# Kernel optimization log

Measured on AMD Instinct MI355X. Metric: run time of the kernel, lower is better.

The kernel has to match this reference:

```python
import jax, jax.numpy as jnp
import numpy as np

BS, C, D = 4096, 16384, 128
POS_ALPHA, POS_DELTA = 32.0, 0.1
NEG_ALPHA, NEG_DELTA = 32.0, -0.1


def _normalize(x):
    # F.normalize(x, dim=1)
    return x / jnp.linalg.norm(x, axis=1, keepdims=True)


def _masked_lse(sims, mask, axis, use_max):
    """Faithful port of Criterion.masked_logsumexp (returns per-entry lse and the
    nonzero-entry mask that torch uses to filter before the final mean)."""
    m = sims * mask
    if use_max:
        ref = jnp.max(m, axis=axis, keepdims=True)
    else:
        ref = jnp.min(m, axis=axis, keepdims=True)
    ref = jax.lax.stop_gradient(ref)  # torch: ref_v.detach()
    # torch: nz_entries = max + min of (sims*mask); keep where nonzero
    nz = (jnp.max(m, axis=axis) + jnp.min(m, axis=axis)) != 0
    s = jnp.sum(jnp.exp(sims - ref) * mask, axis=axis)
    lse = jnp.log(jnp.where(nz, s, 1.0)) + jnp.squeeze(ref, axis=axis)
    return lse, nz


def setup_inputs() -> dict:
    key = jax.random.key(0)
    k1, k2, k3 = jax.random.split(key, 3)
    batch = jax.random.normal(k1, (BS, D), dtype=jnp.float32)
    # proxies = randn/proxy_div, init_dev=0 so no max-shift
    proxies = jax.random.normal(k2, (C, D), dtype=jnp.float32) / 8.0
    labels = jax.random.randint(k3, (BS,), 0, C)
    return {"batch": batch, "proxies": proxies, "labels": labels}


def reference(batch, proxies, labels):
    batch = _normalize(batch)          # [BS, D]
    proxies = _normalize(proxies)      # [C, D]

    pos_sims = batch @ proxies[labels].T   # [BS, BS] cosine sims to positive proxies
    sims = batch @ proxies.T               # [BS, C]

    same = (labels[:, None] == labels[None, :]).astype(batch.dtype)              # [BS, BS]
    diff = (labels[:, None] != jnp.arange(C)[None, :]).astype(batch.dtype)       # [BS, C]

    w_pos = -POS_ALPHA * (pos_sims - POS_DELTA)
    w_neg = NEG_ALPHA * (sims - NEG_DELTA)

    # mode='anchor' -> dim=0; cosine -> max=False for pos, max=True for neg
    pos_lse, pos_nz = _masked_lse(w_pos, same, axis=0, use_max=False)
    neg_lse, neg_nz = _masked_lse(w_neg, diff, axis=0, use_max=True)

    # nca_clean=False -> softplus
    pos_s = jax.nn.softplus(pos_lse)
    neg_s = jax.nn.softplus(neg_lse)

    # torch takes mean only over nz entries
    pos_mean = jnp.sum(jnp.where(pos_nz, pos_s, 0.0)) / jnp.maximum(jnp.sum(pos_nz), 1).astype(batch.dtype)
    neg_mean = jnp.sum(jnp.where(neg_nz, neg_s, 0.0)) / jnp.maximum(jnp.sum(neg_nz), 1).astype(batch.dtype)
    return pos_mean + neg_mean
```

## Files before the change

### kernel.cpp

```cpp
#include <hip/hip_runtime.h>
#include <math.h>

#define BS 4096
#define C_CLS 16384
#define D 128
#define NS 32
#define NR 2
#define KE 46.16624130844683f
#define POS_C 4.616624130844683f
#define LN2 0.69314718055994531f
#define CORR_BLOCKS 256
#define NEG_BLOCKS 2048

typedef __attribute__((ext_vector_type(8))) short short8;
typedef __attribute__((ext_vector_type(4))) float f32x4;

__device__ inline float bf2f(unsigned short h) {
    return __uint_as_float(((unsigned)h) << 16);
}
__device__ inline unsigned short f2bf(float f) {
    unsigned u = __float_as_uint(f);
    u += 0x7FFF + ((u >> 16) & 1);
    return (unsigned short)(u >> 16);
}
__device__ inline float fastexp2(float x) {
    return __int_as_float((int)fmaf(x, 8388608.0f, 1064866816.0f));
}
__device__ inline float softplus(float x) {
    return fmaxf(x, 0.0f) + log1pf(__expf(-fabsf(x)));
}
__device__ inline void gload16(const void* g, void* l) {
    __builtin_amdgcn_global_load_lds((const __attribute__((address_space(1))) void*)g,
                                     (__attribute__((address_space(3))) void*)l, 16, 0, 0);
}
__device__ inline unsigned fenc(float f) {
    unsigned u = __float_as_uint(f);
    return (u & 0x80000000u) ? ~u : (u | 0x80000000u);
}
__device__ inline float fdec(unsigned k) {
    return (k & 0x80000000u) ? __uint_as_float(k ^ 0x80000000u) : __uint_as_float(~k);
}

__global__ __launch_bounds__(256) void normalize_all(const float* __restrict__ batch,
                                                     const float* __restrict__ proxies,
                                                     short* __restrict__ bbf,
                                                     short* __restrict__ pbf,
                                                     float* __restrict__ acc,
                                                     float* __restrict__ negSub,
                                                     float* __restrict__ posSum,
                                                     float* __restrict__ posCnt,
                                                     unsigned* __restrict__ posMaxK,
                                                     unsigned* __restrict__ posMinK,
                                                     float* __restrict__ negAcc,
                                                     int* __restrict__ counter) {
    const int sub = threadIdx.x >> 5;
    const int lane32 = threadIdx.x & 31;
    const int row = blockIdx.x * 8 + sub;
    const bool isb = row < BS;
    const float* src = isb ? batch : proxies;
    short* dst = isb ? bbf : pbf;
    const int r = isb ? row : row - BS;
    const float sc = isb ? 1.0f : KE;

    float4 v = ((const float4*)(src + (size_t)r * D))[lane32];
    float ss = v.x * v.x + v.y * v.y + v.z * v.z + v.w * v.w;
#pragma unroll
    for (int off = 16; off; off >>= 1) ss += __shfl_xor(ss, off);
    float inv = rsqrtf(ss) * sc;
    ushort4 o;
    o.x = f2bf(v.x * inv);
    o.y = f2bf(v.y * inv);
    o.z = f2bf(v.z * inv);
    o.w = f2bf(v.w * inv);
    ((ushort4*)(dst + (size_t)r * D))[lane32] = o;

    const int bid = blockIdx.x, t = threadIdx.x;
    if (bid < 64) negSub[bid * 256 + t] = 0.0f;
    else if (bid < 128) posSum[(bid - 64) * 256 + t] = 0.0f;
    else if (bid < 192) posCnt[(bid - 128) * 256 + t] = 0.0f;
    else if (bid < 256) posMaxK[(bid - 192) * 256 + t] = 0u;
    else if (bid < 320) posMinK[(bid - 256) * 256 + t] = 0xFFFFFFFFu;
    else if (bid < 384) negAcc[(bid - 320) * 256 + t] = 0.0f;
    if (bid == 0 && t == 0) *counter = 0;
}

__global__ __launch_bounds__(256) void mm_all(const short* __restrict__ pbf,
                                              const short* __restrict__ bbf,
                                              const int* __restrict__ labels,
                                              float* __restrict__ negSub,
                                              float* __restrict__ posSum,
                                              float* __restrict__ posCnt,
                                              unsigned* __restrict__ posMaxK,
                                              unsigned* __restrict__ posMinK,
                                              float* __restrict__ negAcc) {
    __shared__ short8 frag[2][16 * 64];

    const int bid = blockIdx.x;
    const int tid = threadIdx.x;
    const int w = tid >> 6, lane = tid & 63, l16 = lane & 15, g = lane >> 4;

    if (bid < CORR_BLOCKS) {
        const int ibase = bid * 16 + w * 4;
        int lab[4];
        float d[4];
#pragma unroll
        for (int r = 0; r < 4; r++) {
            const int i = ibase + r;
            lab[r] = labels[i];
            ushort2 av = ((const ushort2*)(bbf + (size_t)i * D))[lane];
            ushort2 pv = ((const ushort2*)(pbf + (size_t)lab[r] * D))[lane];
            d[r] = bf2f(av.x) * bf2f(pv.x) + bf2f(av.y) * bf2f(pv.y);
        }
#pragma unroll
        for (int off = 32; off; off >>= 1)
#pragma unroll
            for (int r = 0; r < 4; r++) d[r] += __shfl_xor(d[r], off);

        if (lane == 0) {
#pragma unroll
            for (int r = 0; r < 4; r++) {
                atomicAdd(&negSub[lab[r]], fastexp2(d[r]));
                atomicAdd(&posSum[lab[r]], fastexp2(POS_C - d[r]));
                atomicAdd(&posCnt[lab[r]], 1.0f);
                unsigned k = fenc(fmaf(d[r], -LN2, 3.2f));
                atomicMax(&posMaxK[lab[r]], k);
                atomicMin(&posMinK[lab[r]], k);
            }
        }
        return;
    }

    const int n = bid - CORR_BLOCKS;
    const int pg = (n & 7) * 8 + ((n >> 3) & 7);
    const int sp = n >> 6;
    const int wbase = pg * 256 + w * 64;

    short8 a[4][4];
#pragma unroll
    for (int pt = 0; pt < 4; pt++)
#pragma unroll
        for (int kk = 0; kk < 4; kk++)
            a[pt][kk] = *(const short8*)(pbf + (size_t)(wbase + pt * 16 + l16) * D + kk * 32 + g * 8);

    float s[4][4];
#pragma unroll
    for (int pt = 0; pt < 4; pt++)
#pragma unroll
        for (int r = 0; r < 4; r++) s[pt][r] = 0.0f;

    const int ibeg = sp * (BS / NS);
    const short* srcbase = bbf + (size_t)(ibeg + w * 16 + l16) * D + g * 8;

#define STAGE(rr)                                                            \
    {                                                                        \
        const short* sn_ = srcbase + (size_t)(rr) * 64 * D;                  \
        _Pragma("unroll") for (int kk = 0; kk < 4; kk++)                     \
            gload16(sn_ + kk * 32, &frag[(rr) & 1][(w * 4 + kk) * 64]);      \
    }

    STAGE(0)
    asm volatile("s_waitcnt vmcnt(0)" ::: "memory");
    __syncthreads();

#pragma unroll
    for (int rnd = 0; rnd < NR; rnd++) {
        if (rnd + 1 < NR) STAGE(rnd + 1)

        const short8* fb = &frag[rnd & 1][0];
#pragma unroll
        for (int bt = 0; bt < 4; bt++) {
            short8 b[4];
#pragma unroll
            for (int kk = 0; kk < 4; kk++) b[kk] = fb[(bt * 4 + kk) * 64 + lane];
#pragma unroll
            for (int pt = 0; pt < 4; pt++) {
                f32x4 acc = {0.0f, 0.0f, 0.0f, 0.0f};
#pragma unroll
                for (int kk = 0; kk < 4; kk++)
                    acc = __builtin_amdgcn_mfma_f32_16x16x32_bf16(a[pt][kk], b[kk], acc, 0, 0, 0);
#pragma unroll
                for (int r = 0; r < 4; r++) s[pt][r] += fastexp2(acc[r]);
            }
        }
        asm volatile("s_waitcnt vmcnt(0)" ::: "memory");
        __syncthreads();
    }
#undef STAGE

#pragma unroll
    for (int off = 1; off < 16; off <<= 1)
#pragma unroll
        for (int pt = 0; pt < 4; pt++)
#pragma unroll
            for (int r = 0; r < 4; r++) s[pt][r] += __shfl_xor(s[pt][r], off);

    if (l16 == 0) {
#pragma unroll
        for (int pt = 0; pt < 4; pt++)
#pragma unroll
            for (int r = 0; r < 4; r++)
                atomicAdd(&negAcc[wbase + pt * 16 + g * 4 + r], s[pt][r]);
    }
}

__global__ __launch_bounds__(256) void final_reduce(const float* __restrict__ negAcc,
                                                    const float* __restrict__ negSub,
                                                    const int* __restrict__ labels,
                                                    const float* __restrict__ posSum,
                                                    const float* __restrict__ posCnt,
                                                    const unsigned* __restrict__ posMaxK,
                                                    const unsigned* __restrict__ posMinK,
                                                    float* __restrict__ acc,
                                                    int* __restrict__ counter,
                                                    float* __restrict__ out) {
    const int n = blockIdx.x * 256 + threadIdx.x;
    float add = 0.0f, cnt = 0.0f;
    int slot;
    if (n < C_CLS) {
        slot = 2;
        float s = fmaxf(negAcc[n] - negSub[n], 1e-30f);
        add = softplus(logf(s) + 3.2f);
        cnt = 1.0f;
    } else {
        slot = 0;
        const int j = n - C_CLS;
        const int lab = labels[j];
        float s = posSum[lab], c = posCnt[lab];
        float mxw = fdec(posMaxK[lab]), mnw = fdec(posMinK[lab]);
        float maxm = (c < (float)BS) ? fmaxf(mxw, 0.0f) : mxw;
        float minm = (c < (float)BS) ? fminf(mnw, 0.0f) : mnw;
        bool nz = (maxm + minm) != 0.0f;
        if (nz) {
            add = softplus(logf(s));
            cnt = 1.0f;
        }
    }
#pragma unroll
    for (int off = 32; off; off >>= 1) {
        add += __shfl_xor(add, off);
        cnt += __shfl_xor(cnt, off);
    }
    if ((threadIdx.x & 63) == 0) {
        atomicAdd(&acc[slot], add);
        atomicAdd(&acc[slot + 1], cnt);
    }

    __shared__ int amLast;
    __threadfence();
    if (threadIdx.x == 0) amLast = (atomicAdd(counter, 1) == (int)gridDim.x - 1);
    __syncthreads();
    if (amLast && threadIdx.x == 0) {
        __threadfence();
        out[0] = acc[0] / fmaxf(acc[1], 1.0f) + acc[2] / fmaxf(acc[3], 1.0f);
    }
}

extern "C" void kernel_launch(void* const* d_in, const int* in_sizes, int n_in,
                              void* d_out, int out_size, void* d_ws, size_t ws_size,
                              hipStream_t stream) {
    const float* batch = (const float*)d_in[0];
    const float* proxies = (const float*)d_in[1];
    const int* labels = (const int*)d_in[2];
    float* out = (float*)d_out;

    char* ws = (char*)d_ws;
    float* acc = (float*)ws;
    int* counter = (int*)(ws + 64);
    short* bbf = (short*)(ws + 256);
    short* pbf = (short*)(ws + 256 + (size_t)BS * D * 2);
    char* p = ws + 256 + (size_t)(BS + C_CLS) * D * 2;
    float* negSub = (float*)p;        p += (size_t)C_CLS * 4;
    float* posSum = (float*)p;        p += (size_t)C_CLS * 4;
    float* posCnt = (float*)p;        p += (size_t)C_CLS * 4;
    unsigned* posMaxK = (unsigned*)p; p += (size_t)C_CLS * 4;
    unsigned* posMinK = (unsigned*)p; p += (size_t)C_CLS * 4;
    float* negAcc = (float*)p;

    normalize_all<<<(BS + C_CLS) / 8, 256, 0, stream>>>(batch, proxies, bbf, pbf, acc,
                                                        negSub, posSum, posCnt, posMaxK,
                                                        posMinK, negAcc, counter);
    mm_all<<<CORR_BLOCKS + NEG_BLOCKS, 256, 0, stream>>>(pbf, bbf, labels, negSub,
                                                         posSum, posCnt, posMaxK,
                                                         posMinK, negAcc);
    final_reduce<<<(C_CLS + BS) / 256, 256, 0, stream>>>(negAcc, negSub, labels, posSum,
                                                         posCnt, posMaxK, posMinK,
                                                         acc, counter, out);
}
```

Baseline: 51.63 us.

## Replace atomic neg accumulation with per-split partial buffer and fewer, longer blocks

The batch dimension in the negative-sum GEMM is split into 8 slices instead of 32, so each block loops over 8 staged rounds and there are 512 negative blocks instead of 2048. Each slice now writes its per-class partial exp-sums to its own row of a partial buffer instead of using global atomicAdd. The final reduce kernel sums the 8 partials per class. This removes atomic contention and the zero-init of the accumulator, and amortizes the A-fragment loads over more rounds. The cost is fewer blocks to fill the GPU and a non-unrolled round loop.

```diff
diff --git a/kernel.cpp b/kernel.cpp
--- a/kernel.cpp
+++ b/kernel.cpp
@@ -4,13 +4,13 @@
 #define BS 4096
 #define C_CLS 16384
 #define D 128
-#define NS 32
-#define NR 2
+#define NS 8
+#define NR 8
 #define KE 46.16624130844683f
 #define POS_C 4.616624130844683f
 #define LN2 0.69314718055994531f
 #define CORR_BLOCKS 256
-#define NEG_BLOCKS 2048
+#define NEG_BLOCKS 512
 
 typedef __attribute__((ext_vector_type(8))) short short8;
 typedef __attribute__((ext_vector_type(4))) float f32x4;
@@ -51,7 +51,6 @@
                                                      float* __restrict__ posCnt,
                                                      unsigned* __restrict__ posMaxK,
                                                      unsigned* __restrict__ posMinK,
-                                                     float* __restrict__ negAcc,
                                                      int* __restrict__ counter) {
     const int sub = threadIdx.x >> 5;
     const int lane32 = threadIdx.x & 31;
@@ -80,19 +79,18 @@
     else if (bid < 192) posCnt[(bid - 128) * 256 + t] = 0.0f;
     else if (bid < 256) posMaxK[(bid - 192) * 256 + t] = 0u;
     else if (bid < 320) posMinK[(bid - 256) * 256 + t] = 0xFFFFFFFFu;
-    else if (bid < 384) negAcc[(bid - 320) * 256 + t] = 0.0f;
     if (bid == 0 && t == 0) *counter = 0;
 }
 
 __global__ __launch_bounds__(256) void mm_all(const short* __restrict__ pbf,
                                               const short* __restrict__ bbf,
                                               const int* __restrict__ labels,
+                                              float* __restrict__ S,
                                               float* __restrict__ negSub,
                                               float* __restrict__ posSum,
                                               float* __restrict__ posCnt,
                                               unsigned* __restrict__ posMaxK,
-                                              unsigned* __restrict__ posMinK,
-                                              float* __restrict__ negAcc) {
+                                              unsigned* __restrict__ posMinK) {
     __shared__ short8 frag[2][16 * 64];
 
     const int bid = blockIdx.x;
@@ -162,11 +160,11 @@
     asm volatile("s_waitcnt vmcnt(0)" ::: "memory");
     __syncthreads();
 
-#pragma unroll
     for (int rnd = 0; rnd < NR; rnd++) {
+        const int cur = rnd & 1;
         if (rnd + 1 < NR) STAGE(rnd + 1)
 
-        const short8* fb = &frag[rnd & 1][0];
+        const short8* fb = &frag[cur][0];
 #pragma unroll
         for (int bt = 0; bt < 4; bt++) {
             short8 b[4];
@@ -198,12 +196,14 @@
 #pragma unroll
         for (int pt = 0; pt < 4; pt++)
 #pragma unroll
-            for (int r = 0; r < 4; r++)
-                atomicAdd(&negAcc[wbase + pt * 16 + g * 4 + r], s[pt][r]);
-    }
-}
-
-__global__ __launch_bounds__(256) void final_reduce(const float* __restrict__ negAcc,
+            for (int r = 0; r < 4; r++) {
+                int row = wbase + pt * 16 + g * 4 + r;
+                S[(size_t)sp * C_CLS + row] = s[pt][r];
+            }
+    }
+}
+
+__global__ __launch_bounds__(256) void final_reduce(const float* __restrict__ S,
                                                     const float* __restrict__ negSub,
                                                     const int* __restrict__ labels,
                                                     const float* __restrict__ posSum,
@@ -218,7 +218,10 @@
     int slot;
     if (n < C_CLS) {
         slot = 2;
-        float s = fmaxf(negAcc[n] - negSub[n], 1e-30f);
+        float s = 0.0f;
+#pragma unroll
+        for (int p = 0; p < NS; p++) s += S[(size_t)p * C_CLS + n];
+        s = fmaxf(s - negSub[n], 1e-30f);
         add = softplus(logf(s) + 3.2f);
         cnt = 1.0f;
     } else {
@@ -269,20 +272,19 @@
     short* bbf = (short*)(ws + 256);
     short* pbf = (short*)(ws + 256 + (size_t)BS * D * 2);
     char* p = ws + 256 + (size_t)(BS + C_CLS) * D * 2;
+    float* negS = (float*)p;          p += (size_t)C_CLS * NS * 4;
     float* negSub = (float*)p;        p += (size_t)C_CLS * 4;
     float* posSum = (float*)p;        p += (size_t)C_CLS * 4;
     float* posCnt = (float*)p;        p += (size_t)C_CLS * 4;
     unsigned* posMaxK = (unsigned*)p; p += (size_t)C_CLS * 4;
-    unsigned* posMinK = (unsigned*)p; p += (size_t)C_CLS * 4;
-    float* negAcc = (float*)p;
+    unsigned* posMinK = (unsigned*)p;
 
     normalize_all<<<(BS + C_CLS) / 8, 256, 0, stream>>>(batch, proxies, bbf, pbf, acc,
                                                         negSub, posSum, posCnt, posMaxK,
-                                                        posMinK, negAcc, counter);
-    mm_all<<<CORR_BLOCKS + NEG_BLOCKS, 256, 0, stream>>>(pbf, bbf, labels, negSub,
-                                                         posSum, posCnt, posMaxK,
-                                                         posMinK, negAcc);
-    final_reduce<<<(C_CLS + BS) / 256, 256, 0, stream>>>(negAcc, negSub, labels, posSum,
+                                                        posMinK, counter);
+    mm_all<<<CORR_BLOCKS + NEG_BLOCKS, 256, 0, stream>>>(pbf, bbf, labels, negS, negSub,
+                                                         posSum, posCnt, posMaxK, posMinK);
+    final_reduce<<<(C_CLS + BS) / 256, 256, 0, stream>>>(negS, negSub, labels, posSum,
                                                          posCnt, posMaxK, posMinK,
                                                          acc, counter, out);
 }
```

Measured after the change: 45.94 us. 1.12x faster.
